# Kernel optimization log

Hardware: AMD Instinct MI355X
Metric: run time of the kernel (lower is better)

## Reference

```python
import jax, jax.numpy as jnp
import numpy as np

# db4 reconstruction filters (pywt convention): rec_lo = reversed(dec_lo),
# rec_hi[k] = (-1)^k * dec_lo[k]
REC_LO = [0.23037781330885523, 0.7148465705525415, 0.6308807679295904,
          -0.02798376941698385, -0.18703481171888114, 0.030841381835986965,
          0.032883011666982945, -0.010597401784997278]
REC_HI = [-0.010597401784997278, -0.032883011666982945, 0.030841381835986965,
          0.18703481171888114, -0.02798376941698385, -0.6308807679295904,
          0.7148465705525415, -0.23037781330885523]
FILT_LEN = 8


def _idwt1d(cA, cD, axis):
    """Periodized single-level inverse DWT along `axis`. N -> 2N."""
    cA = jnp.moveaxis(cA, axis, -1)
    cD = jnp.moveaxis(cD, axis, -1)
    N = cA.shape[-1]
    up_a = jnp.zeros(cA.shape[:-1] + (2 * N,), cA.dtype).at[..., ::2].set(cA)
    up_d = jnp.zeros(cD.shape[:-1] + (2 * N,), cD.dtype).at[..., ::2].set(cD)
    # circular synthesis: y[m] = sum_k g[k]*up_a[m-k] + h[k]*up_d[m-k]
    y = sum(REC_LO[k] * jnp.roll(up_a, k, axis=-1) +
            REC_HI[k] * jnp.roll(up_d, k, axis=-1) for k in range(FILT_LEN))
    y = jnp.roll(y, -(FILT_LEN - 2), axis=-1)  # phase alignment (periodization)
    return jnp.moveaxis(y, -1, axis)


def setup_inputs() -> dict:
    key = jax.random.key(0)
    x = jax.random.normal(key, (64, 256, 256, 16), dtype=jnp.float32)
    return {"x": x}


def reference(x):
    # x: [B, H, W, 4*C] with channel groups = (cA, cH, cV, cD)
    c = x.shape[-1] // 4
    cA, cH, cV, cD = (x[..., :c], x[..., c:2 * c],
                      x[..., 2 * c:3 * c], x[..., 3 * c:])
    lo = _idwt1d(cA, cH, axis=1)   # [B, 2H, W, C]
    hi = _idwt1d(cV, cD, axis=1)   # [B, 2H, W, C]
    return _idwt1d(lo, hi, axis=2)  # [B, 2H, 2W, C]
```

## Files before the change

kernel.cpp:

```cpp
#include <hip/hip_runtime.h>


#define N 256
#define RJ 16

typedef float f32x4 __attribute__((ext_vector_type(4)));

#define LGKM_BARRIER()                                   \
  do {                                                   \
    asm volatile("s_waitcnt lgkmcnt(0)" ::: "memory");   \
    __builtin_amdgcn_s_barrier();                        \
    asm volatile("" ::: "memory");                       \
  } while (0)

__device__ __forceinline__ f32x4 fma4v(const f32x4 acc, const float s,
                                       const f32x4 a) {
  const f32x4 sv = {s, s, s, s};
  return __builtin_elementwise_fma(a, sv, acc);
}

__device__ __forceinline__ f32x4 shflxor1(const f32x4 v) {
  f32x4 r;
  r.x = __shfl_xor(v.x, 1);
  r.y = __shfl_xor(v.y, 1);
  r.z = __shfl_xor(v.z, 1);
  r.w = __shfl_xor(v.w, 1);
  return r;
}

__global__ __launch_bounds__(512, 4) void idwt2_sep19_kernel(
    const float* __restrict__ x, float* __restrict__ out) {
  constexpr float LO[8] = {
      0.23037781330885523f,  0.7148465705525415f,  0.6308807679295904f,
      -0.02798376941698385f, -0.18703481171888114f, 0.030841381835986965f,
      0.032883011666982945f, -0.010597401784997278f};
  constexpr float HIW[8] = {
      -0.010597401784997278f, -0.032883011666982945f, 0.030841381835986965f,
      0.18703481171888114f,  -0.02798376941698385f,  -0.6308807679295904f,
      0.7148465705525415f,   -0.23037781330885523f};
  const float Lw[2][4] = {{LO[6], LO[4], LO[2], LO[0]},
                          {LO[7], LO[5], LO[3], LO[1]}};
  const float Hw[2][4] = {{HIW[6], HIW[4], HIW[2], HIW[0]},
                          {HIW[7], HIW[5], HIW[3], HIW[1]}};

  __shared__ f32x4 I[2][4][258];

  const int t = threadIdx.x;
  const int bx = blockIdx.x;
  const int b = bx >> 4;
  const int r0 = (bx & 15) * RJ;

  const f32x4* xb = reinterpret_cast<const f32x4*>(x) + (size_t)b * N * N * 4;
  f32x4* ob = reinterpret_cast<f32x4*>(out) + (size_t)b * (2 * N) * (2 * N);

  const int f = t & 3;
  const int p = t >> 2;
  const bool fo = f & 1;

  float w_own[4], w_opp[4];
#pragma unroll
  for (int s = 0; s < 4; ++s) {
    w_own[s] = fo ? Hw[1][s] : Lw[0][s];
    w_opp[s] = fo ? Hw[0][s] : Lw[1][s];
  }

  f32x4 w0[4], w1[4], n0, n1;
  auto ldrow = [&](int lr, f32x4& A, f32x4& B) {
    const int gr = (r0 + lr) & (N - 1);
    const f32x4* xrow = xb + (size_t)gr * (N * 4);
    A = xrow[t];
    B = xrow[t + 512];
  };

  auto p1 = [&](int j, int buf) {
    f32x4 sAo = {0.f, 0.f, 0.f, 0.f}, sAx = {0.f, 0.f, 0.f, 0.f};
    f32x4 sBo = {0.f, 0.f, 0.f, 0.f}, sBx = {0.f, 0.f, 0.f, 0.f};
#pragma unroll
    for (int sy = 0; sy < 4; ++sy) {
      const f32x4 a = w0[(j + sy) & 3];
      const f32x4 bb = w1[(j + sy) & 3];
      sAo = fma4v(sAo, w_own[sy], a);
      sAx = fma4v(sAx, w_opp[sy], a);
      sBo = fma4v(sBo, w_own[sy], bb);
      sBx = fma4v(sBx, w_opp[sy], bb);
    }
    const f32x4 vA = sAo + shflxor1(sAx);
    const f32x4 vB = sBo + shflxor1(sBx);
    I[buf][f][p] = vA;
    I[buf][f][p + 128] = vB;
  };

#pragma unroll
  for (int m = 0; m < 4; ++m) ldrow(m, w0[m], w1[m]);
  ldrow(4, n0, n1);
  p1(0, 0);
  w0[0] = n0;
  w1[0] = n1;
  ldrow(5, n0, n1);
  LGKM_BARRIER();

  const int jx = t >> 1;
  const int q = t & 1;
  float Lq[4], Hq[4];
#pragma unroll
  for (int s = 0; s < 4; ++s) {
    Lq[s] = q ? Lw[1][s] : Lw[0][s];
    Hq[s] = q ? Hw[1][s] : Hw[0][s];
  }

#pragma unroll
  for (int c = 0; c < RJ; ++c) {
    const int buf = c & 1;

    f32x4 o0 = {0.f, 0.f, 0.f, 0.f};
    f32x4 o1 = {0.f, 0.f, 0.f, 0.f};
#pragma unroll
    for (int s = 0; s < 4; ++s) {
      const int xc = (jx + s) & (N - 1);
      o0 = fma4v(o0, Lq[s], I[buf][0][xc]);
      o0 = fma4v(o0, Hq[s], I[buf][2][xc]);
      o1 = fma4v(o1, Lq[s], I[buf][1][xc]);
      o1 = fma4v(o1, Hq[s], I[buf][3][xc]);
    }
    const int jy = r0 + c;
    f32x4* po = ob + (size_t)(2 * jy) * (2 * N) + t;
    po[0] = o0;
    po[2 * N] = o1;

    if (c < RJ - 1) {
      p1(c + 1, buf ^ 1);
      if (c <= RJ - 3) {
        w0[(c + 1) & 3] = n0;
        w1[(c + 1) & 3] = n1;
      }
      if (c <= RJ - 4) ldrow(c + 6, n0, n1);
      LGKM_BARRIER();
    }
  }
}

extern "C" void kernel_launch(void* const* d_in, const int* in_sizes, int n_in,
                              void* d_out, int out_size, void* d_ws,
                              size_t ws_size, hipStream_t stream) {
  const float* x = reinterpret_cast<const float*>(d_in[0]);
  float* out = reinterpret_cast<float*>(d_out);
  const int grid = 64 * (N / RJ);
  idwt2_sep19_kernel<<<grid, 512, 0, stream>>>(x, out);
}
```

Before: 107.1 us.

## Process two rows per barrier and store intermediate LDS tiles as bf16

The main loop now handles two output row pairs per iteration, which halves the number of block barriers and doubles the prefetch depth of global row loads. The intermediate vertical-pass results in shared memory are packed to bf16 so two rows fit in the double buffer without growing LDS use. This is meant to cut barrier stalls and improve load overlap. The cost is reduced precision of the intermediate values plus extra pack and unpack instructions.

```diff
diff --git a/kernel.cpp b/kernel.cpp
--- a/kernel.cpp
+++ b/kernel.cpp
@@ -1,8 +1,10 @@
 #include <hip/hip_runtime.h>
+#include <hip/hip_bf16.h>
 
 
 #define N 256
 #define RJ 16
+#define NC (RJ / 2)
 
 typedef float f32x4 __attribute__((ext_vector_type(4)));
 
@@ -28,7 +30,25 @@
   return r;
 }
 
-__global__ __launch_bounds__(512, 4) void idwt2_sep19_kernel(
+__device__ __forceinline__ uint2 pack_bf16x4(const f32x4 v) {
+  __hip_bfloat162 lo = __float22bfloat162_rn(make_float2(v.x, v.y));
+  __hip_bfloat162 hi = __float22bfloat162_rn(make_float2(v.z, v.w));
+  uint2 r;
+  r.x = *reinterpret_cast<const unsigned int*>(&lo);
+  r.y = *reinterpret_cast<const unsigned int*>(&hi);
+  return r;
+}
+
+__device__ __forceinline__ f32x4 unpack_bf16x4(const uint2 u) {
+  f32x4 r;
+  r.x = __uint_as_float(u.x << 16);
+  r.y = __uint_as_float(u.x & 0xffff0000u);
+  r.z = __uint_as_float(u.y << 16);
+  r.w = __uint_as_float(u.y & 0xffff0000u);
+  return r;
+}
+
+__global__ __launch_bounds__(512, 4) void idwt2_sep21_kernel(
     const float* __restrict__ x, float* __restrict__ out) {
   constexpr float LO[8] = {
       0.23037781330885523f,  0.7148465705525415f,  0.6308807679295904f,
@@ -43,7 +63,7 @@
   const float Hw[2][4] = {{HIW[6], HIW[4], HIW[2], HIW[0]},
                           {HIW[7], HIW[5], HIW[3], HIW[1]}};
 
-  __shared__ f32x4 I[2][4][258];
+  __shared__ uint2 I[2][2][4][258];
 
   const int t = threadIdx.x;
   const int bx = blockIdx.x;
@@ -64,7 +84,8 @@
     w_opp[s] = fo ? Hw[0][s] : Lw[1][s];
   }
 
-  f32x4 w0[4], w1[4], n0, n1;
+  f32x4 w0[4], w1[4];
+  f32x4 nA0, nB0, nA1, nB1;
   auto ldrow = [&](int lr, f32x4& A, f32x4& B) {
     const int gr = (r0 + lr) & (N - 1);
     const f32x4* xrow = xb + (size_t)gr * (N * 4);
@@ -72,7 +93,7 @@
     B = xrow[t + 512];
   };
 
-  auto p1 = [&](int j, int buf) {
+  auto p1 = [&](int j, int buf, int r) {
     f32x4 sAo = {0.f, 0.f, 0.f, 0.f}, sAx = {0.f, 0.f, 0.f, 0.f};
     f32x4 sBo = {0.f, 0.f, 0.f, 0.f}, sBx = {0.f, 0.f, 0.f, 0.f};
 #pragma unroll
@@ -86,17 +107,22 @@
     }
     const f32x4 vA = sAo + shflxor1(sAx);
     const f32x4 vB = sBo + shflxor1(sBx);
-    I[buf][f][p] = vA;
-    I[buf][f][p + 128] = vB;
+    I[buf][r][f][p] = pack_bf16x4(vA);
+    I[buf][r][f][p + 128] = pack_bf16x4(vB);
   };
 
 #pragma unroll
   for (int m = 0; m < 4; ++m) ldrow(m, w0[m], w1[m]);
-  ldrow(4, n0, n1);
-  p1(0, 0);
-  w0[0] = n0;
-  w1[0] = n1;
-  ldrow(5, n0, n1);
+  ldrow(4, nA0, nB0);
+  ldrow(5, nA1, nB1);
+  p1(0, 0, 0);
+  w0[0] = nA0;
+  w1[0] = nB0;
+  p1(1, 0, 1);
+  w0[1] = nA1;
+  w1[1] = nB1;
+  ldrow(6, nA0, nB0);
+  ldrow(7, nA1, nB1);
   LGKM_BARRIER();
 
   const int jx = t >> 1;
@@ -109,31 +135,38 @@
   }
 
 #pragma unroll
-  for (int c = 0; c < RJ; ++c) {
+  for (int c = 0; c < NC; ++c) {
     const int buf = c & 1;
 
-    f32x4 o0 = {0.f, 0.f, 0.f, 0.f};
-    f32x4 o1 = {0.f, 0.f, 0.f, 0.f};
 #pragma unroll
-    for (int s = 0; s < 4; ++s) {
-      const int xc = (jx + s) & (N - 1);
-      o0 = fma4v(o0, Lq[s], I[buf][0][xc]);
-      o0 = fma4v(o0, Hq[s], I[buf][2][xc]);
-      o1 = fma4v(o1, Lq[s], I[buf][1][xc]);
-      o1 = fma4v(o1, Hq[s], I[buf][3][xc]);
+    for (int r = 0; r < 2; ++r) {
+      f32x4 o0 = {0.f, 0.f, 0.f, 0.f};
+      f32x4 o1 = {0.f, 0.f, 0.f, 0.f};
+#pragma unroll
+      for (int s = 0; s < 4; ++s) {
+        const int xc = (jx + s) & (N - 1);
+        o0 = fma4v(o0, Lq[s], unpack_bf16x4(I[buf][r][0][xc]));
+        o0 = fma4v(o0, Hq[s], unpack_bf16x4(I[buf][r][2][xc]));
+        o1 = fma4v(o1, Lq[s], unpack_bf16x4(I[buf][r][1][xc]));
+        o1 = fma4v(o1, Hq[s], unpack_bf16x4(I[buf][r][3][xc]));
+      }
+      const int jy = r0 + 2 * c + r;
+      f32x4* po = ob + (size_t)(2 * jy) * (2 * N) + t;
+      po[0] = o0;
+      po[2 * N] = o1;
     }
-    const int jy = r0 + c;
-    f32x4* po = ob + (size_t)(2 * jy) * (2 * N) + t;
-    po[0] = o0;
-    po[2 * N] = o1;
 
-    if (c < RJ - 1) {
-      p1(c + 1, buf ^ 1);
-      if (c <= RJ - 3) {
-        w0[(c + 1) & 3] = n0;
-        w1[(c + 1) & 3] = n1;
+    if (c < NC - 1) {
+      p1(2 * c + 2, buf ^ 1, 0);
+      w0[(2 * c + 2) & 3] = nA0;
+      w1[(2 * c + 2) & 3] = nB0;
+      p1(2 * c + 3, buf ^ 1, 1);
+      if (c < NC - 2) {
+        w0[(2 * c + 3) & 3] = nA1;
+        w1[(2 * c + 3) & 3] = nB1;
+        ldrow(2 * c + 8, nA0, nB0);
+        ldrow(2 * c + 9, nA1, nB1);
       }
-      if (c <= RJ - 4) ldrow(c + 6, n0, n1);
       LGKM_BARRIER();
     }
   }
@@ -145,5 +178,5 @@
   const float* x = reinterpret_cast<const float*>(d_in[0]);
   float* out = reinterpret_cast<float*>(d_out);
   const int grid = 64 * (N / RJ);
-  idwt2_sep19_kernel<<<grid, 512, 0, stream>>>(x, out);
+  idwt2_sep21_kernel<<<grid, 512, 0, stream>>>(x, out);
 }
```

Result: no change. 108.7 us (+1.4%).
